# Kernel tuning notes

Measured on AMD Instinct MI355X. Metric: run time of the kernel, lower is better.

The kernel has to match this reference:

```python
import jax, jax.numpy as jnp
import numpy as np

N = 8192          # rays
T = 256           # num_steps (default in run())
GEO = 15          # geo_feat dim (density hidden width 16 -> sigma + 15 feats)
CLIPD = 32        # clip feature dim
BOUND = 1.0
MIN_NEAR = 0.2
DENSITY_SCALE = 1.0


def setup_inputs() -> dict:
    key = jax.random.key(0)
    ks = jax.random.split(key, 16)
    # ray origins inside the AABB [-1,1]^3, directions unit-normalized
    rays_o = (jax.random.uniform(ks[0], (N, 3)) - 0.5) * 1.0
    rd = jax.random.normal(ks[1], (N, 3))
    rays_d = rd / jnp.linalg.norm(rd, axis=-1, keepdims=True)
    direction_norms = 1.0 + 0.5 * jax.random.uniform(ks[2], (N,))
    s = 0.1  # weight scale keeps exp(sigma-logit) in a sane range
    params = dict(
        Wd1=jax.random.normal(ks[3], (3, 64)) * s,   bd1=jnp.zeros((64,)),
        Wd2=jax.random.normal(ks[4], (64, 16)) * s,  bd2=jnp.zeros((16,)),
        Wc1=jax.random.normal(ks[5], (18, 64)) * s,  bc1=jnp.zeros((64,)),
        Wc2=jax.random.normal(ks[6], (64, 3)) * s,   bc2=jnp.zeros((3,)),
        Wk1=jax.random.normal(ks[7], (16, 64)) * s,  bk1=jnp.zeros((64,)),
        Wk2=jax.random.normal(ks[8], (64, CLIPD)) * s, bk2=jnp.zeros((CLIPD,)),
    )
    return dict(rays_o=rays_o, rays_d=rays_d, direction_norms=direction_norms, **params)


def reference(rays_o, rays_d, direction_norms,
              Wd1, bd1, Wd2, bd2, Wc1, bc1, Wc2, bc2, Wk1, bk1, Wk2, bk2):
    aabb_min = jnp.full((3,), -BOUND, rays_o.dtype)
    aabb_max = jnp.full((3,), BOUND, rays_o.dtype)

    # --- near_far_from_aabb (slab test, clamped to min_near) ---
    inv_d = 1.0 / rays_d
    t1 = (aabb_min - rays_o) * inv_d
    t2 = (aabb_max - rays_o) * inv_d
    nears = jnp.maximum(jnp.minimum(t1, t2).max(-1), MIN_NEAR)   # (N,)
    fars = jnp.maximum(jnp.maximum(t1, t2).min(-1), nears + 1e-4)

    # --- stratified-uniform z samples (perturb=False) ---
    z = jnp.linspace(0.0, 1.0, T, dtype=rays_o.dtype)
    z_vals = nears[:, None] + (fars - nears)[:, None] * z        # (N,T)
    sample_dist = (fars - nears) / T                              # (N,)

    xyzs = rays_o[:, None, :] + rays_d[:, None, :] * z_vals[..., None]  # (N,T,3)
    xyzs = jnp.clip(xyzs, aabb_min, aabb_max)

    # --- density MLP: sigma = exp(h0), geo_feat = h[1:] ---
    h = jax.nn.relu(jnp.einsum('ntc,ch->nth', xyzs, Wd1) + bd1)
    h = jnp.einsum('nth,hk->ntk', h, Wd2) + bd2                   # (N,T,16)
    sigma = jnp.exp(h[..., 0])                                    # (N,T)
    geo_feat = h[..., 1:]                                         # (N,T,GEO)

    # --- alpha compositing weights ---
    deltas = jnp.concatenate(
        [z_vals[:, 1:] - z_vals[:, :-1], sample_dist[:, None]], axis=-1)  # (N,T)
    alphas = 1.0 - jnp.exp(-deltas * DENSITY_SCALE * sigma)
    alphas_shifted = jnp.concatenate(
        [jnp.ones_like(alphas[:, :1]), 1.0 - alphas + 1e-15], axis=-1)
    trans = jnp.cumprod(alphas_shifted, axis=-1)[:, :-1]          # transmittance
    weights = alphas * trans                                      # (N,T)
    mask = weights > 1e-4

    # --- color MLP on (dir, geo_feat); unmasked points stay zero ---
    dirs = jnp.broadcast_to(rays_d[:, None, :], xyzs.shape)
    cin = jnp.concatenate([dirs, geo_feat], axis=-1)              # (N,T,18)
    hc = jax.nn.relu(jnp.einsum('ntc,ch->nth', cin, Wc1) + bc1)
    rgbs = jax.nn.sigmoid(jnp.einsum('nth,hk->ntk', hc, Wc2) + bc2)
    rgbs = jnp.where(mask[..., None], rgbs, 0.0)                  # (N,T,3)

    weights = jnp.where(mask, weights, 0.0)
    weights_sum = weights.sum(-1)                                 # (N,)
    depth = (weights * z_vals).sum(-1) / direction_norms          # (N,)
    depth_variance = jax.lax.stop_gradient(
        (weights * (depth[:, None] - z_vals / direction_norms[:, None]) ** 2).sum(-1))
    coordinates_map = (weights[..., None] * xyzs).sum(-2)         # (N,3)
    image = (weights[..., None] * rgbs).sum(-2)                   # (N,3)
    image = image + (1.0 - weights_sum)[:, None] * 1.0            # white bg

    # --- clip MLP on (geo_feat, sigma), composited with detached weights ---
    kin = jnp.concatenate([geo_feat, sigma[..., None]], axis=-1)  # (N,T,16)
    hk = jax.nn.relu(jnp.einsum('ntc,ch->nth', kin, Wk1) + bk1)
    clip_feats = jnp.einsum('nth,hk->ntk', hk, Wk2) + bk2         # (N,T,CLIPD)
    clip_features = (jax.lax.stop_gradient(weights)[..., None] * clip_feats).sum(-2)

    return (image, depth, depth_variance, coordinates_map, rgbs, clip_features)
```

## Files before the change

kernel.cpp:

```cpp
#include <hip/hip_runtime.h>

#define NRAYS 8192
typedef const float* fpp;
typedef unsigned int uint;

typedef short bf16x8 __attribute__((ext_vector_type(8)));
typedef int   i32x4  __attribute__((ext_vector_type(4)));
typedef int   i32x2  __attribute__((ext_vector_type(2)));
typedef float f32x4  __attribute__((ext_vector_type(4)));

__device__ __forceinline__ uint bfbits(float f) {
  uint u = __float_as_uint(f);
  return (u + 0x7FFFu + ((u >> 16) & 1u)) >> 16;
}
__device__ __forceinline__ short f2bf(float f) { return (short)bfbits(f); }
__device__ __forceinline__ int pk2(float a, float b) {
  return (int)(bfbits(a) | (bfbits(b) << 16));
}
__device__ __forceinline__ int cvtpk(float a, float b) {
  int r;
  asm("v_cvt_pk_bf16_f32 %0, %1, %2" : "=v"(r) : "v"(a), "v"(b));
  return r;
}
__device__ __forceinline__ f32x4 MFMA(bf16x8 a, bf16x8 b, f32x4 c) {
  return __builtin_amdgcn_mfma_f32_16x16x32_bf16(a, b, c, 0, 0, 0);
}
__device__ __forceinline__ float waveAllSum(float v) {
#pragma unroll
  for (int off = 32; off > 0; off >>= 1) v += __shfl_xor(v, off, 64);
  return v;
}

#define OFF_IMG   0
#define OFF_DEPTH 24576
#define OFF_VAR   32768
#define OFF_COORD 40960
#define OFF_RGBS  65536
#define OFF_CLIP  6356992

__device__ __forceinline__ int pi_row(int t, int m) {
  int a = m >> 2, r = m & 3;
  return (t < 2) ? (8 * a + 4 * t + r) : (32 + 8 * a + 4 * (t - 2) + r);
}

__global__ void prep_kernel(fpp Wd2, fpp Wc1, fpp Wk1, fpp Wc2, fpp bc1, fpp bk1,
                            uint4* ws) {
  const int lane = threadIdx.x & 63;
  const int c16 = lane & 15, o = lane >> 4;
  uint t[4];
#pragma unroll
  for (int kt = 0; kt < 2; kt++) {
#pragma unroll
    for (int q = 0; q < 4; q++) {
      float w0 = Wd2[(32 * kt + 8 * o + 2 * q) * 16 + c16];
      float w1 = Wd2[(32 * kt + 8 * o + 2 * q + 1) * 16 + c16];
      t[q] = ((uint)(unsigned short)f2bf(w1) << 16) | (uint)(unsigned short)f2bf(w0);
    }
    ws[lane * 2 + kt] = make_uint4(t[0], t[1], t[2], t[3]);
  }
#pragma unroll
  for (int ht = 0; ht < 4; ht++) {
    uint tc[4], tk[4];
    const int hc_ = pi_row(ht, c16);
    const int hk_ = 16 * ht + c16;
#pragma unroll
    for (int q = 0; q < 4; q++) {
      uint pc = 0, pkk = 0;
#pragma unroll
      for (int half = 0; half < 2; half++) {
        int k = 8 * o + 2 * q + half;
        float wc = 0.f, wk = 0.f;
        if (k >= 1 && k <= 15) wc = Wc1[(k + 2) * 64 + hc_];
        else if (k >= 16 && k <= 18) wc = Wc1[(k - 16) * 64 + hc_];
        else if (k == 19) wc = bc1[hc_];
        if (k == 0) wk = Wk1[15 * 64 + hk_];
        else if (k <= 15) wk = Wk1[(k - 1) * 64 + hk_];
        else if (k == 16) wk = bk1[hk_];
        pc  |= (uint)(unsigned short)f2bf(wc) << (16 * half);
        pkk |= (uint)(unsigned short)f2bf(wk) << (16 * half);
      }
      tc[q] = pc; tk[q] = pkk;
    }
    ws[128 + lane * 4 + ht] = make_uint4(tc[0], tc[1], tc[2], tc[3]);
    ws[384 + lane * 4 + ht] = make_uint4(tk[0], tk[1], tk[2], tk[3]);
  }
#pragma unroll
  for (int kt = 0; kt < 2; kt++) {
#pragma unroll
    for (int q = 0; q < 4; q++) {
      uint p = 0;
#pragma unroll
      for (int half = 0; half < 2; half++) {
        int h = 32 * kt + 8 * o + 2 * q + half;
        float w = (c16 < 3) ? Wc2[h * 3 + c16] : 0.f;
        p |= (uint)(unsigned short)f2bf(w) << (16 * half);
      }
      t[q] = p;
    }
    ws[640 + lane * 2 + kt] = make_uint4(t[0], t[1], t[2], t[3]);
  }
}

template <bool PREP>
__global__ __launch_bounds__(256, 4) void nerf_kernel(
    fpp rays_o, fpp rays_d, fpp dnorms,
    fpp Wd1, fpp bd1, fpp Wd2, fpp bd2,
    fpp Wc1, fpp bc1, fpp Wc2, fpp bc2,
    fpp Wk1, fpp bk1, fpp Wk2, fpp bk2,
    const uint4* wsp, float* out)
{
  __shared__ short  geoA[4][256][8];
  __shared__ short  geoB[4][256][8];
  __shared__ float  tmp[4][256];
  __shared__ i32x4  slots4[4][4];

  const int tid = threadIdx.x;
  const int wave = tid >> 6, lane = tid & 63;
  const int c16 = lane & 15, o = lane >> 4;
  const int ray = blockIdx.x * 4 + wave;

  const float ox = rays_o[ray * 3 + 0], oy = rays_o[ray * 3 + 1], oz = rays_o[ray * 3 + 2];
  const float dx = rays_d[ray * 3 + 0], dy = rays_d[ray * 3 + 1], dz = rays_d[ray * 3 + 2];
  const float dn = dnorms[ray];
  const float ixr = 1.f / dx, iyr = 1.f / dy, izr = 1.f / dz;
  float t1x = (-1.f - ox) * ixr, t2x = (1.f - ox) * ixr;
  float t1y = (-1.f - oy) * iyr, t2y = (1.f - oy) * iyr;
  float t1z = (-1.f - oz) * izr, t2z = (1.f - oz) * izr;
  float nearv = fmaxf(fmaxf(fminf(t1x, t2x), fminf(t1y, t2y)), fminf(t1z, t2z));
  nearv = fmaxf(nearv, 0.2f);
  float farv = fminf(fminf(fmaxf(t1x, t2x), fmaxf(t1y, t2y)), fmaxf(t1z, t2z));
  farv = fmaxf(farv, nearv + 0.0001f);
  const float span = farv - nearv;

  bf16x8 a2[2], c1a[4], k1a[4], argb[2];
  if (PREP) {
#pragma unroll
    for (int kt = 0; kt < 2; kt++) {
      a2[kt]   = __builtin_bit_cast(bf16x8, wsp[lane * 2 + kt]);
      argb[kt] = __builtin_bit_cast(bf16x8, wsp[640 + lane * 2 + kt]);
    }
#pragma unroll
    for (int ht = 0; ht < 4; ht++) {
      c1a[ht] = __builtin_bit_cast(bf16x8, wsp[128 + lane * 4 + ht]);
      k1a[ht] = __builtin_bit_cast(bf16x8, wsp[384 + lane * 4 + ht]);
    }
  } else {
#pragma unroll
    for (int kt = 0; kt < 2; kt++)
#pragma unroll
      for (int j = 0; j < 8; j++) {
        a2[kt][j]   = f2bf(Wd2[(32 * kt + 8 * o + j) * 16 + c16]);
        argb[kt][j] = (c16 < 3) ? f2bf(Wc2[(32 * kt + 8 * o + j) * 3 + c16]) : (short)0;
      }
#pragma unroll
    for (int ht = 0; ht < 4; ht++) {
      const int hc_ = pi_row(ht, c16);
      const int hk_ = 16 * ht + c16;
#pragma unroll
      for (int j = 0; j < 8; j++) {
        int k = 8 * o + j;
        float wc = 0.f, wk = 0.f;
        if (k >= 1 && k <= 15) wc = Wc1[(k + 2) * 64 + hc_];
        else if (k >= 16 && k <= 18) wc = Wc1[(k - 16) * 64 + hc_];
        else if (k == 19) wc = bc1[hc_];
        if (k == 0) wk = Wk1[15 * 64 + hk_];
        else if (k <= 15) wk = Wk1[(k - 1) * 64 + hk_];
        else if (k == 16) wk = bk1[hk_];
        c1a[ht][j] = f2bf(wc);
        k1a[ht][j] = f2bf(wk);
      }
    }
  }

  float p1[16], q1[16];
#pragma unroll
  for (int kt = 0; kt < 2; kt++)
#pragma unroll
    for (int j = 0; j < 8; j++) {
      int h = 32 * kt + 8 * o + j;
      float w0 = Wd1[h], w1 = Wd1[64 + h], w2 = Wd1[128 + h];
      p1[8 * kt + j] = fmaf(w0, ox, fmaf(w1, oy, fmaf(w2, oz, bd1[h])));
      q1[8 * kt + j] = fmaf(w0, dx, fmaf(w1, dy, w2 * dz));
    }
  f32x4 bd2v = {bd2[4 * o], bd2[4 * o + 1], bd2[4 * o + 2], bd2[4 * o + 3]};
  f32x4 bc2i = {0.f, 0.f, 0.f, 0.f};
  if (o == 0) { bc2i[0] = bc2[0]; bc2i[1] = bc2[1]; bc2i[2] = bc2[2]; }
  const f32x4 zacc = {0.f, 0.f, 0.f, 0.f};

  short* gws = ((o < 2) ? &geoA[wave][0][4 * o] : &geoB[wave][0][4 * (o - 2)]) + c16 * 8;
  float* tpw = &tmp[wave][c16];
  float zt = nearv + span * ((float)c16 * (1.f / 255.f));
  const float ztstep = span * (16.f / 255.f);
#pragma unroll 2
  for (int mt = 0; mt < 16; mt++) {
    bf16x8 h1f[2];
#pragma unroll
    for (int kt = 0; kt < 2; kt++) {
      i32x4 tv;
#pragma unroll
      for (int q = 0; q < 4; q++) {
        float a = fmaxf(fmaf(q1[8 * kt + 2 * q],     zt, p1[8 * kt + 2 * q]),     0.f);
        float b = fmaxf(fmaf(q1[8 * kt + 2 * q + 1], zt, p1[8 * kt + 2 * q + 1]), 0.f);
        tv[q] = cvtpk(a, b);
      }
      h1f[kt] = __builtin_bit_cast(bf16x8, tv);
    }
    f32x4 acc = bd2v;
    acc = MFMA(a2[0], h1f[0], acc);
    acc = MFMA(a2[1], h1f[1], acc);
    float sgm = __expf(acc[0]);
    i32x2 pkv;
    pkv[0] = pk2((o == 0) ? sgm : acc[0], acc[1]);
    pkv[1] = pk2(acc[2], acc[3]);
    *(i32x2*)gws = pkv;
    if (o == 0) *tpw = sgm;
    gws += 128; tpw += 16; zt += ztstep;
  }

  float z[4], wm[4];
  float ws, swz, depth, var, cx, cy, cz;
  {
    f32x4 sgv = *(f32x4*)&tmp[wave][lane * 4];
    float alpha[4], v[4], m[4];
#pragma unroll
    for (int i = 0; i < 4; i++) {
      int t = lane * 4 + i;
      z[i] = nearv + span * ((float)t * (1.f / 255.f));
      float delta = (t < 255) ? span * (1.f / 255.f) : span * (1.f / 256.f);
      alpha[i] = 1.f - __expf(-delta * sgv[i]);
      v[i] = 1.f - alpha[i] + 1e-15f;
    }
    m[0] = 1.f; m[1] = v[0]; m[2] = m[1] * v[1]; m[3] = m[2] * v[2];
    float ip = m[3] * v[3];
#pragma unroll
    for (int off = 1; off < 64; off <<= 1) {
      float u = __shfl_up(ip, off, 64);
      if (lane >= off) ip *= u;
    }
    float E = __shfl_up(ip, 1, 64);
    if (lane == 0) E = 1.f;
    ws = 0.f; swz = 0.f; cx = 0.f; cy = 0.f; cz = 0.f;
#pragma unroll
    for (int i = 0; i < 4; i++) {
      float w = alpha[i] * (E * m[i]);
      wm[i] = (w > 0.0001f) ? w : 0.f;
      ws += wm[i];
      swz = fmaf(wm[i], z[i], swz);
      float xc = fminf(fmaxf(fmaf(dx, z[i], ox), -1.f), 1.f);
      float yc = fminf(fmaxf(fmaf(dy, z[i], oy), -1.f), 1.f);
      float zc = fminf(fmaxf(fmaf(dz, z[i], oz), -1.f), 1.f);
      cx = fmaf(wm[i], xc, cx); cy = fmaf(wm[i], yc, cy); cz = fmaf(wm[i], zc, cz);
    }
    f32x4 wv4 = {wm[0], wm[1], wm[2], wm[3]};
    *(f32x4*)&tmp[wave][lane * 4] = wv4;
    ws = waveAllSum(ws); swz = waveAllSum(swz);
    cx = waveAllSum(cx); cy = waveAllSum(cy); cz = waveAllSum(cz);
    depth = swz / dn;
    var = 0.f;
#pragma unroll
    for (int i = 0; i < 4; i++) {
      float dd = depth - z[i] / dn;
      var = fmaf(wm[i], dd * dd, var);
    }
    var = waveAllSum(var);
  }
  if (lane == 0) {
    out[OFF_DEPTH + ray] = depth;
    out[OFF_VAR + ray]   = var;
    out[OFF_COORD + ray * 3 + 0] = cx;
    out[OFF_COORD + ray * 3 + 1] = cy;
    out[OFF_COORD + ray * 3 + 2] = cz;
    i32x4 dv; dv[0] = pk2(dx, dy); dv[1] = pk2(dz, 1.f); dv[2] = 0; dv[3] = 0;
    slots4[wave][0] = dv;
    i32x4 kv; kv[0] = 0x3F80; kv[1] = 0; kv[2] = 0; kv[3] = 0;
    slots4[wave][1] = kv;
    i32x4 zv = {0, 0, 0, 0};
    slots4[wave][2] = zv;
  }
  __syncthreads();

  float ia0 = 0.f, ia1 = 0.f, ia2 = 0.f;
  float gp[4][4];
#pragma unroll
  for (int ht = 0; ht < 4; ht++)
#pragma unroll
    for (int r = 0; r < 4; r++) gp[ht][r] = 0.f;

  const short* pB0 = (o == 0) ? &geoA[wave][0][0]
                   : (o == 1) ? &geoB[wave][0][0]
                   : (o == 2) ? (const short*)&slots4[wave][0]
                              : (const short*)&slots4[wave][2];
  const short* pK0 = (o == 0) ? &geoA[wave][0][0]
                   : (o == 1) ? &geoB[wave][0][0]
                   : (o == 2) ? (const short*)&slots4[wave][1]
                              : (const short*)&slots4[wave][2];
  const int sstep = (o < 2) ? 8 : 0;
  const short* pBs = pB0 + c16 * sstep;
  const short* pKs = pK0 + c16 * sstep;
  const int stepB = 16 * sstep;
  const float* tpr = &tmp[wave][c16];

  bf16x8 bcur = *(const bf16x8*)pBs;
  bf16x8 kcur = *(const bf16x8*)pKs;
  float  wcur = *tpr;

#pragma unroll 2
  for (int mt = 0; mt < 16; mt++) {
    const short* pBn = (mt < 15) ? (pBs + stepB) : pBs;
    const short* pKn = (mt < 15) ? (pKs + stepB) : pKs;
    const float* tpn = (mt < 15) ? (tpr + 16) : tpr;
    bf16x8 bnxt = *(const bf16x8*)pBn;
    bf16x8 knxt = *(const bf16x8*)pKn;
    float  wnxt = *tpn;

    const bf16x8 bfr1 = bcur;
    const bf16x8 kfr  = kcur;
    const float  wmv  = wcur;
    i32x4 h0v, h1v;
#pragma unroll
    for (int ht = 0; ht < 4; ht++) {
      f32x4 hc = MFMA(c1a[ht], bfr1, zacc);
      int u0 = cvtpk(fmaxf(hc[0], 0.f), fmaxf(hc[1], 0.f));
      int u1 = cvtpk(fmaxf(hc[2], 0.f), fmaxf(hc[3], 0.f));
      if (ht == 0)      { h0v[0] = u0; h0v[1] = u1; }
      else if (ht == 1) { h0v[2] = u0; h0v[3] = u1; }
      else if (ht == 2) { h1v[0] = u0; h1v[1] = u1; }
      else              { h1v[2] = u0; h1v[3] = u1; }
    }
    f32x4 racc = bc2i;
    racc = MFMA(argb[0], __builtin_bit_cast(bf16x8, h0v), racc);
    racc = MFMA(argb[1], __builtin_bit_cast(bf16x8, h1v), racc);
    if (o == 0) {
      const int s = mt * 16 + c16;
      const long ro = OFF_RGBS + ((long)ray * 256 + s) * 3;
      float s0 = __builtin_amdgcn_rcpf(1.f + __expf(-racc[0]));
      float s1 = __builtin_amdgcn_rcpf(1.f + __expf(-racc[1]));
      float s2 = __builtin_amdgcn_rcpf(1.f + __expf(-racc[2]));
      const bool mk = (wmv > 0.f);
      s0 = mk ? s0 : 0.f; s1 = mk ? s1 : 0.f; s2 = mk ? s2 : 0.f;
      out[ro + 0] = s0; out[ro + 1] = s1; out[ro + 2] = s2;
      ia0 = fmaf(wmv, s0, ia0);
      ia1 = fmaf(wmv, s1, ia1);
      ia2 = fmaf(wmv, s2, ia2);
    }
#pragma unroll
    for (int ht = 0; ht < 4; ht++) {
      f32x4 hk = MFMA(k1a[ht], kfr, zacc);
#pragma unroll
      for (int r = 0; r < 4; r++)
        gp[ht][r] = fmaf(wmv, fmaxf(hk[r], 0.f), gp[ht][r]);
    }
    bcur = bnxt; kcur = knxt; wcur = wnxt;
    pBs = pBn; pKs = pKn; tpr = tpn;
  }

#pragma unroll
  for (int off = 1; off < 16; off <<= 1) {
    ia0 += __shfl_xor(ia0, off, 64);
    ia1 += __shfl_xor(ia1, off, 64);
    ia2 += __shfl_xor(ia2, off, 64);
  }
  if (lane == 0) {
    out[OFF_IMG + ray * 3 + 0] = ia0 + (1.f - ws);
    out[OFF_IMG + ray * 3 + 1] = ia1 + (1.f - ws);
    out[OFF_IMG + ray * 3 + 2] = ia2 + (1.f - ws);
  }

#pragma unroll
  for (int ht = 0; ht < 4; ht++)
#pragma unroll
    for (int r = 0; r < 4; r++) {
      float g = gp[ht][r];
      g += __shfl_xor(g, 1, 64); g += __shfl_xor(g, 2, 64);
      g += __shfl_xor(g, 4, 64); g += __shfl_xor(g, 8, 64);
      gp[ht][r] = g;
    }
  {
    const int k2 = 2 * c16;
    const float2* w2 = (const float2*)Wk2;
    float cp0 = 0.f, cp1 = 0.f;
#pragma unroll
    for (int ht = 0; ht < 4; ht++)
#pragma unroll
      for (int r = 0; r < 4; r++) {
        int h = 16 * ht + 4 * o + r;
        float2 wv = w2[h * 16 + c16];
        cp0 = fmaf(gp[ht][r], wv.x, cp0);
        cp1 = fmaf(gp[ht][r], wv.y, cp1);
      }
    cp0 += __shfl_xor(cp0, 16, 64); cp0 += __shfl_xor(cp0, 32, 64);
    cp1 += __shfl_xor(cp1, 16, 64); cp1 += __shfl_xor(cp1, 32, 64);
    cp0 = fmaf(ws, bk2[k2], cp0);
    cp1 = fmaf(ws, bk2[k2 + 1], cp1);
    if (lane < 16) {
      out[OFF_CLIP + ray * 32 + k2]     = cp0;
      out[OFF_CLIP + ray * 32 + k2 + 1] = cp1;
    }
  }
}

extern "C" void kernel_launch(void* const* d_in, const int* in_sizes, int n_in,
                              void* d_out, int out_size, void* d_ws, size_t ws_size,
                              hipStream_t stream) {
  const bool prep = (ws_size >= 12288);
  if (prep) {
    prep_kernel<<<1, 64, 0, stream>>>((fpp)d_in[5], (fpp)d_in[7], (fpp)d_in[11],
                                      (fpp)d_in[9], (fpp)d_in[8], (fpp)d_in[12],
                                      (uint4*)d_ws);
    nerf_kernel<true><<<NRAYS / 4, 256, 0, stream>>>(
        (fpp)d_in[0], (fpp)d_in[1], (fpp)d_in[2],
        (fpp)d_in[3], (fpp)d_in[4], (fpp)d_in[5], (fpp)d_in[6],
        (fpp)d_in[7], (fpp)d_in[8], (fpp)d_in[9], (fpp)d_in[10],
        (fpp)d_in[11], (fpp)d_in[12], (fpp)d_in[13], (fpp)d_in[14],
        (const uint4*)d_ws, (float*)d_out);
  } else {
    nerf_kernel<false><<<NRAYS / 4, 256, 0, stream>>>(
        (fpp)d_in[0], (fpp)d_in[1], (fpp)d_in[2],
        (fpp)d_in[3], (fpp)d_in[4], (fpp)d_in[5], (fpp)d_in[6],
        (fpp)d_in[7], (fpp)d_in[8], (fpp)d_in[9], (fpp)d_in[10],
        (fpp)d_in[11], (fpp)d_in[12], (fpp)d_in[13], (fpp)d_in[14],
        (const uint4*)d_ws, (float*)d_out);
  }
}
```

Before: 152.1 us.

## Share one B operand for color and clip MLPs; spread RGB sigmoid across lane groups

Moves the clip-MLP bias row to slot 19 so the color and clip first-layer MFMAs can read the same B fragment, dropping the separate slot and second LDS load per step. Rearranges the Wc2 A-matrix rows so each of the three RGB outputs lands in accumulator element 0 of a different lane group. Each lane then computes one sigmoid instead of one lane group computing all three, spreading the exp/rcp work and the RGB stores across the wave. It also removes the software prefetch and sets unroll 1 on both loops, which may expose LDS latency but reduces register pressure.

```diff
diff --git a/kernel.cpp b/kernel.cpp
--- a/kernel.cpp
+++ b/kernel.cpp
@@ -75,7 +75,7 @@
         else if (k == 19) wc = bc1[hc_];
         if (k == 0) wk = Wk1[15 * 64 + hk_];
         else if (k <= 15) wk = Wk1[(k - 1) * 64 + hk_];
-        else if (k == 16) wk = bk1[hk_];
+        else if (k == 19) wk = bk1[hk_];
         pc  |= (uint)(unsigned short)f2bf(wc) << (16 * half);
         pkk |= (uint)(unsigned short)f2bf(wk) << (16 * half);
       }
@@ -92,7 +92,10 @@
 #pragma unroll
       for (int half = 0; half < 2; half++) {
         int h = 32 * kt + 8 * o + 2 * q + half;
-        float w = (c16 < 3) ? Wc2[h * 3 + c16] : 0.f;
+        float w = 0.f;
+        if (c16 == 0)      w = Wc2[h * 3 + 0];
+        else if (c16 == 4) w = Wc2[h * 3 + 1];
+        else if (c16 == 8) w = Wc2[h * 3 + 2];
         p |= (uint)(unsigned short)f2bf(w) << (16 * half);
       }
       t[q] = p;
@@ -149,8 +152,13 @@
     for (int kt = 0; kt < 2; kt++)
 #pragma unroll
       for (int j = 0; j < 8; j++) {
-        a2[kt][j]   = f2bf(Wd2[(32 * kt + 8 * o + j) * 16 + c16]);
-        argb[kt][j] = (c16 < 3) ? f2bf(Wc2[(32 * kt + 8 * o + j) * 3 + c16]) : (short)0;
+        a2[kt][j] = f2bf(Wd2[(32 * kt + 8 * o + j) * 16 + c16]);
+        int h = 32 * kt + 8 * o + j;
+        float w = 0.f;
+        if (c16 == 0)      w = Wc2[h * 3 + 0];
+        else if (c16 == 4) w = Wc2[h * 3 + 1];
+        else if (c16 == 8) w = Wc2[h * 3 + 2];
+        argb[kt][j] = f2bf(w);
       }
 #pragma unroll
     for (int ht = 0; ht < 4; ht++) {
@@ -165,7 +173,7 @@
         else if (k == 19) wc = bc1[hc_];
         if (k == 0) wk = Wk1[15 * 64 + hk_];
         else if (k <= 15) wk = Wk1[(k - 1) * 64 + hk_];
-        else if (k == 16) wk = bk1[hk_];
+        else if (k == 19) wk = bk1[hk_];
         c1a[ht][j] = f2bf(wc);
         k1a[ht][j] = f2bf(wk);
       }
@@ -184,14 +192,14 @@
     }
   f32x4 bd2v = {bd2[4 * o], bd2[4 * o + 1], bd2[4 * o + 2], bd2[4 * o + 3]};
   f32x4 bc2i = {0.f, 0.f, 0.f, 0.f};
-  if (o == 0) { bc2i[0] = bc2[0]; bc2i[1] = bc2[1]; bc2i[2] = bc2[2]; }
+  if (o < 3) bc2i[0] = bc2[o];
   const f32x4 zacc = {0.f, 0.f, 0.f, 0.f};
 
   short* gws = ((o < 2) ? &geoA[wave][0][4 * o] : &geoB[wave][0][4 * (o - 2)]) + c16 * 8;
   float* tpw = &tmp[wave][c16];
   float zt = nearv + span * ((float)c16 * (1.f / 255.f));
   const float ztstep = span * (16.f / 255.f);
-#pragma unroll 2
+#pragma unroll 1
   for (int mt = 0; mt < 16; mt++) {
     bf16x8 h1f[2];
 #pragma unroll
@@ -272,54 +280,36 @@
     out[OFF_COORD + ray * 3 + 2] = cz;
     i32x4 dv; dv[0] = pk2(dx, dy); dv[1] = pk2(dz, 1.f); dv[2] = 0; dv[3] = 0;
     slots4[wave][0] = dv;
-    i32x4 kv; kv[0] = 0x3F80; kv[1] = 0; kv[2] = 0; kv[3] = 0;
-    slots4[wave][1] = kv;
     i32x4 zv = {0, 0, 0, 0};
     slots4[wave][2] = zv;
   }
   __syncthreads();
 
-  float ia0 = 0.f, ia1 = 0.f, ia2 = 0.f;
+  float ia = 0.f;
   float gp[4][4];
 #pragma unroll
   for (int ht = 0; ht < 4; ht++)
 #pragma unroll
     for (int r = 0; r < 4; r++) gp[ht][r] = 0.f;
 
-  const short* pB0 = (o == 0) ? &geoA[wave][0][0]
-                   : (o == 1) ? &geoB[wave][0][0]
-                   : (o == 2) ? (const short*)&slots4[wave][0]
-                              : (const short*)&slots4[wave][2];
-  const short* pK0 = (o == 0) ? &geoA[wave][0][0]
-                   : (o == 1) ? &geoB[wave][0][0]
-                   : (o == 2) ? (const short*)&slots4[wave][1]
-                              : (const short*)&slots4[wave][2];
+  const short* pBs = ((o == 0) ? &geoA[wave][0][0]
+                    : (o == 1) ? &geoB[wave][0][0]
+                    : (o == 2) ? (const short*)&slots4[wave][0]
+                               : (const short*)&slots4[wave][2]);
   const int sstep = (o < 2) ? 8 : 0;
-  const short* pBs = pB0 + c16 * sstep;
-  const short* pKs = pK0 + c16 * sstep;
+  pBs += c16 * sstep;
   const int stepB = 16 * sstep;
   const float* tpr = &tmp[wave][c16];
-
-  bf16x8 bcur = *(const bf16x8*)pBs;
-  bf16x8 kcur = *(const bf16x8*)pKs;
-  float  wcur = *tpr;
-
-#pragma unroll 2
+  float* rgbp = out + OFF_RGBS + (long)ray * 768 + c16 * 3 + o;
+
+#pragma unroll 1
   for (int mt = 0; mt < 16; mt++) {
-    const short* pBn = (mt < 15) ? (pBs + stepB) : pBs;
-    const short* pKn = (mt < 15) ? (pKs + stepB) : pKs;
-    const float* tpn = (mt < 15) ? (tpr + 16) : tpr;
-    bf16x8 bnxt = *(const bf16x8*)pBn;
-    bf16x8 knxt = *(const bf16x8*)pKn;
-    float  wnxt = *tpn;
-
-    const bf16x8 bfr1 = bcur;
-    const bf16x8 kfr  = kcur;
-    const float  wmv  = wcur;
+    const bf16x8 bfr = *(const bf16x8*)pBs;
+    const float wmv = *tpr;
     i32x4 h0v, h1v;
 #pragma unroll
     for (int ht = 0; ht < 4; ht++) {
-      f32x4 hc = MFMA(c1a[ht], bfr1, zacc);
+      f32x4 hc = MFMA(c1a[ht], bfr, zacc);
       int u0 = cvtpk(fmaxf(hc[0], 0.f), fmaxf(hc[1], 0.f));
       int u1 = cvtpk(fmaxf(hc[2], 0.f), fmaxf(hc[3], 0.f));
       if (ht == 0)      { h0v[0] = u0; h0v[1] = u1; }
@@ -330,41 +320,25 @@
     f32x4 racc = bc2i;
     racc = MFMA(argb[0], __builtin_bit_cast(bf16x8, h0v), racc);
     racc = MFMA(argb[1], __builtin_bit_cast(bf16x8, h1v), racc);
-    if (o == 0) {
-      const int s = mt * 16 + c16;
-      const long ro = OFF_RGBS + ((long)ray * 256 + s) * 3;
-      float s0 = __builtin_amdgcn_rcpf(1.f + __expf(-racc[0]));
-      float s1 = __builtin_amdgcn_rcpf(1.f + __expf(-racc[1]));
-      float s2 = __builtin_amdgcn_rcpf(1.f + __expf(-racc[2]));
-      const bool mk = (wmv > 0.f);
-      s0 = mk ? s0 : 0.f; s1 = mk ? s1 : 0.f; s2 = mk ? s2 : 0.f;
-      out[ro + 0] = s0; out[ro + 1] = s1; out[ro + 2] = s2;
-      ia0 = fmaf(wmv, s0, ia0);
-      ia1 = fmaf(wmv, s1, ia1);
-      ia2 = fmaf(wmv, s2, ia2);
+    {
+      float sv = __builtin_amdgcn_rcpf(1.f + __expf(-racc[0]));
+      sv = (wmv > 0.f) ? sv : 0.f;
+      if (o < 3) *rgbp = sv;
+      ia = fmaf(wmv, sv, ia);
     }
 #pragma unroll
     for (int ht = 0; ht < 4; ht++) {
-      f32x4 hk = MFMA(k1a[ht], kfr, zacc);
+      f32x4 hk = MFMA(k1a[ht], bfr, zacc);
 #pragma unroll
       for (int r = 0; r < 4; r++)
         gp[ht][r] = fmaf(wmv, fmaxf(hk[r], 0.f), gp[ht][r]);
     }
-    bcur = bnxt; kcur = knxt; wcur = wnxt;
-    pBs = pBn; pKs = pKn; tpr = tpn;
-  }
-
-#pragma unroll
-  for (int off = 1; off < 16; off <<= 1) {
-    ia0 += __shfl_xor(ia0, off, 64);
-    ia1 += __shfl_xor(ia1, off, 64);
-    ia2 += __shfl_xor(ia2, off, 64);
-  }
-  if (lane == 0) {
-    out[OFF_IMG + ray * 3 + 0] = ia0 + (1.f - ws);
-    out[OFF_IMG + ray * 3 + 1] = ia1 + (1.f - ws);
-    out[OFF_IMG + ray * 3 + 2] = ia2 + (1.f - ws);
-  }
+    pBs += stepB; tpr += 16; rgbp += 48;
+  }
+
+  ia += __shfl_xor(ia, 1, 64); ia += __shfl_xor(ia, 2, 64);
+  ia += __shfl_xor(ia, 4, 64); ia += __shfl_xor(ia, 8, 64);
+  if (c16 == 0 && o < 3) out[OFF_IMG + ray * 3 + o] = ia + (1.f - ws);
 
 #pragma unroll
   for (int ht = 0; ht < 4; ht++)
```

After: 152.4 us. About the same (+0.2%).
